# Optimization experiments

Measured on AMD Instinct MI355X. Metric: run time of the kernel, lower is better.

Reference implementation:

```python
import jax, jax.numpy as jnp
import numpy as np

K = 4096
D = 64
DECAY = 0.99
EPS = 1e-05


def setup_inputs() -> dict:
    key = jax.random.key(0)
    k1, k2 = jax.random.split(key)
    z_e = jax.random.normal(k1, (32, 1024, D), dtype=jnp.float32)
    emb = jax.random.normal(k2, (K, D), dtype=jnp.float32)
    emb = emb / jnp.clip(jnp.linalg.norm(emb, axis=1, keepdims=True), 1e-8)
    return {
        "z_e": z_e,
        "embedding": emb,
        "ema_cluster_size": jnp.zeros((K,), jnp.float32),
        "ema_embedding": jnp.zeros((K, D), jnp.float32),
    }


def reference(z_e, embedding, ema_cluster_size, ema_embedding):
    B, L, Dd = z_e.shape
    flat = z_e.reshape(-1, Dd)                                   # (N, D)
    flat_norm = flat / jnp.clip(jnp.linalg.norm(flat, axis=1, keepdims=True), 1e-8)
    dots = flat_norm @ embedding.T                               # (N, K)
    indices = jnp.argmax(dots, axis=1)                           # (N,)
    z_q = embedding[indices].reshape(B, L, Dd)
    z_q_st = z_e + jax.lax.stop_gradient(z_q - z_e)

    # ---- usage / stats ----
    usage = jnp.zeros((K,), jnp.float32).at[indices].add(1.0)    # bincount
    probs = usage / jnp.maximum(usage.sum(), 1.0)
    safe = jnp.where(probs > 0, probs, 1.0)
    perplexity = jnp.exp(-jnp.sum(probs * jnp.log(safe)))
    dead_ratio = jnp.mean((usage == 0).astype(jnp.float32))
    stats = jnp.stack([perplexity, dead_ratio])

    # ---- EMA update (training-mode buffer math, functional) ----
    fn = jax.lax.stop_gradient(flat_norm)
    embed_sum = jnp.zeros((K, Dd), jnp.float32).at[indices].add(fn)  # one_hot.T @ flat_norm
    new_cs = DECAY * ema_cluster_size + (1.0 - DECAY) * usage
    new_ema_emb = DECAY * ema_embedding + (1.0 - DECAY) * embed_sum
    n = new_cs.sum()
    smoothed = (new_cs + EPS) / (n + K * EPS)
    norm_e = new_ema_emb / jnp.clip(smoothed, EPS)[:, None]
    norm_e = norm_e / jnp.clip(jnp.linalg.norm(norm_e, axis=1, keepdims=True), 1e-8)

    # ---- dead-code reinit (reinit_prob=1.0, threshold=0); deterministic key ----
    N = fn.shape[0]
    rand_idx = jax.random.randint(jax.random.key(1), (K,), 0, N)
    src = fn[rand_idx]
    src = src / jnp.clip(jnp.linalg.norm(src, axis=1, keepdims=True), 1e-8)
    dead = usage <= 0.0
    new_embedding = jnp.where(dead[:, None], src, norm_e)

    return (z_q_st, z_q, indices.reshape(B, L), stats,
            new_embedding, new_cs, new_ema_emb)
```

## Files before the change

### kernel.cpp

```cpp
#include <hip/hip_runtime.h>
#include <math.h>

#define N_TOK 32768
#define KCB   4096
#define SPLITS 6

#define OFF_ZQST   0
#define OFF_ZQ     2097152
#define OFF_IDX    4194304
#define OFF_STATS  4227072
#define OFF_NEWEMB 4227074
#define OFF_NEWCS  4489218
#define OFF_NEWEMA 4493314

#define WS_FN       0
#define WS_ESUM     8388608
#define WS_USAGE    9437184
#define WS_CNTS     9453568
#define WS_FULLKEY  9454592
#define WS_EHI      9716736
#define WS_ELO      10241024
#define WS_PK1      10765312
#define WS_PK2      11551744
#define WS_IDXW     12338176
#define WS_RIDX     12469248
#define WS_FULL     12485632

#define THRKEY 131072u
#define DGRKEY 98304u

typedef __attribute__((ext_vector_type(8))) short short8;
typedef __attribute__((ext_vector_type(4))) float float4v;

__device__ __forceinline__ float wave_sum(float v) {
#pragma unroll
  for (int off = 32; off > 0; off >>= 1) v += __shfl_xor(v, off, 64);
  return v;
}

__device__ __forceinline__ unsigned short f2bf(float f) {
  unsigned u = __float_as_uint(f);
  unsigned r = (u + 0x7fffu + ((u >> 16) & 1u)) >> 16;
  return (unsigned short)r;
}
__device__ __forceinline__ float bf2f(unsigned short h) {
  return __uint_as_float(((unsigned)h) << 16);
}

__device__ __forceinline__ unsigned rotl32(unsigned x, int d) {
  return (x << d) | (x >> (32 - d));
}
__device__ __forceinline__ void tf2x32(unsigned k0, unsigned k1,
                                       unsigned x0, unsigned x1,
                                       unsigned& o0, unsigned& o1) {
  unsigned ks2 = k0 ^ k1 ^ 0x1BD11BDAu;
  unsigned v0 = x0 + k0, v1 = x1 + k1;
  v0 += v1; v1 = rotl32(v1, 13) ^ v0;
  v0 += v1; v1 = rotl32(v1, 15) ^ v0;
  v0 += v1; v1 = rotl32(v1, 26) ^ v0;
  v0 += v1; v1 = rotl32(v1, 6) ^ v0;
  v0 += k1; v1 += ks2 + 1u;
  v0 += v1; v1 = rotl32(v1, 17) ^ v0;
  v0 += v1; v1 = rotl32(v1, 29) ^ v0;
  v0 += v1; v1 = rotl32(v1, 16) ^ v0;
  v0 += v1; v1 = rotl32(v1, 24) ^ v0;
  v0 += ks2; v1 += k0 + 2u;
  v0 += v1; v1 = rotl32(v1, 13) ^ v0;
  v0 += v1; v1 = rotl32(v1, 15) ^ v0;
  v0 += v1; v1 = rotl32(v1, 26) ^ v0;
  v0 += v1; v1 = rotl32(v1, 6) ^ v0;
  v0 += k0; v1 += k1 + 3u;
  v0 += v1; v1 = rotl32(v1, 17) ^ v0;
  v0 += v1; v1 = rotl32(v1, 29) ^ v0;
  v0 += v1; v1 = rotl32(v1, 16) ^ v0;
  v0 += v1; v1 = rotl32(v1, 24) ^ v0;
  v0 += k1; v1 += ks2 + 4u;
  v0 += v1; v1 = rotl32(v1, 13) ^ v0;
  v0 += v1; v1 = rotl32(v1, 15) ^ v0;
  v0 += v1; v1 = rotl32(v1, 26) ^ v0;
  v0 += v1; v1 = rotl32(v1, 6) ^ v0;
  v0 += ks2; v1 += k0 + 5u;
  o0 = v0; o1 = v1;
}

__global__ __launch_bounds__(256) void k_prep(const float* __restrict__ z_e,
                                              const float* __restrict__ emb,
                                              float* __restrict__ fn,
                                              unsigned short* __restrict__ ehi,
                                              unsigned short* __restrict__ elo,
                                              int* __restrict__ ridx,
                                              int* __restrict__ zbase) {
  int b = blockIdx.x;
  int t = threadIdx.x;
  if (b < 8192) {
    int n = b * 4 + (t >> 6);
    int lane = t & 63;
    float x = z_e[n * 64 + lane];
    float ss = wave_sum(x * x);
    fn[n * 64 + lane] = x / fmaxf(sqrtf(ss), 1e-8f);
  } else if (b < 9216) {
    int i = (b - 8192) * 256 + t;
    float x = emb[i];
    unsigned short h = f2bf(x);
    ehi[i] = h;
    elo[i] = f2bf(x - bf2f(h));
  } else if (b < 9224) {
    int j = (b - 9216) * 256 + t;
    unsigned a0, b0, a1, b1;
    tf2x32(0u, 1u, 0u, 2u, a0, b0);
    tf2x32(0u, 1u, 1u, 3u, a1, b1);
    unsigned o0, o1;
    tf2x32(b0, b1, (unsigned)j, (unsigned)(j + 2048), o0, o1);
    ridx[j] = (int)(o0 & 32767u);
    ridx[j + 2048] = (int)(o1 & 32767u);
  } else {
    int i = (b - 9224) * 256 + t;
    zbase[i] = 0;
  }
}

__global__ __launch_bounds__(256, 3) void k_dots(const float* __restrict__ fn,
                                                 const unsigned short* __restrict__ ehi,
                                                 const unsigned short* __restrict__ elo,
                                                 unsigned* __restrict__ pk1,
                                                 unsigned* __restrict__ pk2) {
  int t = threadIdx.x;
  int wave = t >> 6, lane = t & 63;
  int g = lane >> 4, n = lane & 15;
  int qw = blockIdx.x * 256 + wave * 64;
  int split = blockIdx.y;
  int nt16 = (split < 2) ? 704 : 672;
  int tstart16 = (split < 3) ? 704 * split : 672 * split + 64;
  int ntiles = nt16 >> 4;

  short8 ahi[4][2], alo[4][2];
#pragma unroll
  for (int s = 0; s < 4; s++)
#pragma unroll
    for (int ks = 0; ks < 2; ks++) {
      const float* src = fn + (qw + s * 16 + n) * 64 + ks * 32 + g * 8;
      short8 h, l;
#pragma unroll
      for (int j = 0; j < 8; j++) {
        float f = src[j] * 0.125f;
        unsigned short hu = f2bf(f);
        h[j] = (short)hu;
        l[j] = (short)f2bf(f - bf2f(hu));
      }
      ahi[s][ks] = h;
      alo[s][ks] = l;
    }

  unsigned run1[4][4], run2[4][4];
#pragma unroll
  for (int s = 0; s < 4; s++)
#pragma unroll
    for (int r = 0; r < 4; r++) { run1[s][r] = 0u; run2[s][r] = 0u; }

  const unsigned short* bh = ehi + (tstart16 + n) * 64 + g * 8;
  const unsigned short* bl = elo + (tstart16 + n) * 64 + g * 8;
  const float hiclamp = __uint_as_float(0x3F9FFFFFu);

  short8 h0a = *(const short8*)(bh);
  short8 h1a = *(const short8*)(bh + 32);
  short8 l0a = *(const short8*)(bl);
  short8 l1a = *(const short8*)(bl + 32);
  short8 h0b = *(const short8*)(bh + 1024);
  short8 h1b = *(const short8*)(bh + 1024 + 32);
  short8 l0b = *(const short8*)(bl + 1024);
  short8 l1b = *(const short8*)(bl + 1024 + 32);

#define MFMA_BLOCK(H0, H1, L0, L1)                                              \
    float4v a0 = (float4v){1.125f, 1.125f, 1.125f, 1.125f};                     \
    float4v a1 = a0, a2 = a0, a3 = a0;                                          \
    a0 = __builtin_amdgcn_mfma_f32_16x16x32_bf16(alo[0][0], H0, a0, 0, 0, 0);   \
    a1 = __builtin_amdgcn_mfma_f32_16x16x32_bf16(alo[1][0], H0, a1, 0, 0, 0);   \
    a2 = __builtin_amdgcn_mfma_f32_16x16x32_bf16(alo[2][0], H0, a2, 0, 0, 0);   \
    a3 = __builtin_amdgcn_mfma_f32_16x16x32_bf16(alo[3][0], H0, a3, 0, 0, 0);   \
    a0 = __builtin_amdgcn_mfma_f32_16x16x32_bf16(alo[0][1], H1, a0, 0, 0, 0);   \
    a1 = __builtin_amdgcn_mfma_f32_16x16x32_bf16(alo[1][1], H1, a1, 0, 0, 0);   \
    a2 = __builtin_amdgcn_mfma_f32_16x16x32_bf16(alo[2][1], H1, a2, 0, 0, 0);   \
    a3 = __builtin_amdgcn_mfma_f32_16x16x32_bf16(alo[3][1], H1, a3, 0, 0, 0);   \
    a0 = __builtin_amdgcn_mfma_f32_16x16x32_bf16(ahi[0][0], L0, a0, 0, 0, 0);   \
    a1 = __builtin_amdgcn_mfma_f32_16x16x32_bf16(ahi[1][0], L0, a1, 0, 0, 0);   \
    a2 = __builtin_amdgcn_mfma_f32_16x16x32_bf16(ahi[2][0], L0, a2, 0, 0, 0);   \
    a3 = __builtin_amdgcn_mfma_f32_16x16x32_bf16(ahi[3][0], L0, a3, 0, 0, 0);   \
    a0 = __builtin_amdgcn_mfma_f32_16x16x32_bf16(ahi[0][1], L1, a0, 0, 0, 0);   \
    a1 = __builtin_amdgcn_mfma_f32_16x16x32_bf16(ahi[1][1], L1, a1, 0, 0, 0);   \
    a2 = __builtin_amdgcn_mfma_f32_16x16x32_bf16(ahi[2][1], L1, a2, 0, 0, 0);   \
    a3 = __builtin_amdgcn_mfma_f32_16x16x32_bf16(ahi[3][1], L1, a3, 0, 0, 0);   \
    a0 = __builtin_amdgcn_mfma_f32_16x16x32_bf16(ahi[0][0], H0, a0, 0, 0, 0);   \
    a1 = __builtin_amdgcn_mfma_f32_16x16x32_bf16(ahi[1][0], H0, a1, 0, 0, 0);   \
    a2 = __builtin_amdgcn_mfma_f32_16x16x32_bf16(ahi[2][0], H0, a2, 0, 0, 0);   \
    a3 = __builtin_amdgcn_mfma_f32_16x16x32_bf16(ahi[3][0], H0, a3, 0, 0, 0);   \
    a0 = __builtin_amdgcn_mfma_f32_16x16x32_bf16(ahi[0][1], H1, a0, 0, 0, 0);   \
    a1 = __builtin_amdgcn_mfma_f32_16x16x32_bf16(ahi[1][1], H1, a1, 0, 0, 0);   \
    a2 = __builtin_amdgcn_mfma_f32_16x16x32_bf16(ahi[2][1], H1, a2, 0, 0, 0);   \
    a3 = __builtin_amdgcn_mfma_f32_16x16x32_bf16(ahi[3][1], H1, a3, 0, 0, 0);

#define SELECT_BLOCK(KT)                                                        \
    {                                                                           \
      unsigned invb = (unsigned)(nt16 - 1 - (KT) * 16 - n);                     \
      _Pragma("unroll") for (int r = 0; r < 4; r++) {                           \
        float x0 = __builtin_amdgcn_fmed3f(a0[r], 1.0f, hiclamp);               \
        unsigned kb0 = (__float_as_uint(x0) << 10) + invb;                      \
        run2[0][r] = max(run2[0][r], min(run1[0][r], kb0));                     \
        run1[0][r] = max(run1[0][r], kb0);                                      \
        float x1 = __builtin_amdgcn_fmed3f(a1[r], 1.0f, hiclamp);               \
        unsigned kb1 = (__float_as_uint(x1) << 10) + invb;                      \
        run2[1][r] = max(run2[1][r], min(run1[1][r], kb1));                     \
        run1[1][r] = max(run1[1][r], kb1);                                      \
        float x2 = __builtin_amdgcn_fmed3f(a2[r], 1.0f, hiclamp);               \
        unsigned kb2 = (__float_as_uint(x2) << 10) + invb;                      \
        run2[2][r] = max(run2[2][r], min(run1[2][r], kb2));                     \
        run1[2][r] = max(run1[2][r], kb2);                                      \
        float x3 = __builtin_amdgcn_fmed3f(a3[r], 1.0f, hiclamp);               \
        unsigned kb3 = (__float_as_uint(x3) << 10) + invb;                      \
        run2[3][r] = max(run2[3][r], min(run1[3][r], kb3));                     \
        run1[3][r] = max(run1[3][r], kb3);                                      \
      }                                                                         \
    }

#pragma unroll 1
  for (int kt = 0; kt < ntiles; kt += 2) {
    {
      MFMA_BLOCK(h0a, h1a, l0a, l1a)
      int off = (kt + 2) * 1024;
      h0a = *(const short8*)(bh + off);
      h1a = *(const short8*)(bh + off + 32);
      l0a = *(const short8*)(bl + off);
      l1a = *(const short8*)(bl + off + 32);
      SELECT_BLOCK(kt)
    }
    {
      MFMA_BLOCK(h0b, h1b, l0b, l1b)
      int off = (kt + 3) * 1024;
      h0b = *(const short8*)(bh + off);
      h1b = *(const short8*)(bh + off + 32);
      l0b = *(const short8*)(bl + off);
      l1b = *(const short8*)(bl + off + 32);
      SELECT_BLOCK(kt + 1)
    }
  }
#undef MFMA_BLOCK
#undef SELECT_BLOCK

#pragma unroll
  for (int off = 1; off <= 8; off <<= 1) {
#pragma unroll
    for (int s = 0; s < 4; s++)
#pragma unroll
      for (int r = 0; r < 4; r++) {
        unsigned o1 = (unsigned)__shfl_xor((int)run1[s][r], off, 64);
        unsigned o2 = (unsigned)__shfl_xor((int)run2[s][r], off, 64);
        run2[s][r] = max(min(run1[s][r], o1), max(run2[s][r], o2));
        run1[s][r] = max(run1[s][r], o1);
      }
  }

  if (n == 0) {
#pragma unroll
    for (int s = 0; s < 4; s++)
#pragma unroll
      for (int r = 0; r < 4; r++) {
        int q = qw + s * 16 + g * 4 + r;
        pk1[split * N_TOK + q] = run1[s][r];
        pk2[split * N_TOK + q] = run2[s][r];
      }
  }
}

__global__ __launch_bounds__(256) void k_merge_fix(const unsigned* __restrict__ pk1,
                                                   const unsigned* __restrict__ pk2,
                                                   const float* __restrict__ fn,
                                                   const float* __restrict__ emb,
                                                   int* __restrict__ idxw,
                                                   int* __restrict__ cnts,
                                                   int* __restrict__ full,
                                                   unsigned long long* __restrict__ fullkey) {
  __shared__ int nfl;
  __shared__ int fl[256][13];
  int t = threadIdx.x;
  if (t == 0) nfl = 0;
  __syncthreads();
  int q = blockIdx.x * 256 + t;
  unsigned k1v[SPLITS], k2v[SPLITS];
  unsigned b1 = 0u, b2 = 0u;
  int s1 = 0;
#pragma unroll
  for (int s = 0; s < SPLITS; s++) {
    unsigned k1 = pk1[s * N_TOK + q];
    unsigned k2 = pk2[s * N_TOK + q];
    k1v[s] = k1;
    k2v[s] = k2;
    b2 = max(b2, min(b1, k1));
    b2 = max(b2, k2);
    if (k1 > b1) { b1 = k1; s1 = s; }
  }
  int nt16s = (s1 < 2) ? 704 : 672;
  int ts16 = (s1 < 3) ? 704 * s1 : 672 * s1 + 64;
  idxw[q] = ts16 + nt16s - 1 - (int)(b1 & 1023u);
  fullkey[q] = 0ull;
  bool danger = false;
#pragma unroll
  for (int s = 0; s < SPLITS; s++) danger |= (k2v[s] + DGRKEY > b1);
  if (danger) {
    int p = atomicAdd(&cnts[0], 1);
    full[p] = q;
  } else if (b1 - b2 < THRKEY) {
    int p = atomicAdd(&nfl, 1);
    fl[p][0] = q;
#pragma unroll
    for (int s = 0; s < SPLITS; s++) {
      int nt = (s < 2) ? 704 : 672;
      int tss = (s < 3) ? 704 * s : 672 * s + 64;
      fl[p][1 + s] = tss + nt - 1 - (int)(k1v[s] & 1023u);
      fl[p][7 + s] = tss + nt - 1 - (int)(k2v[s] & 1023u);
    }
  }
  __syncthreads();
  int m = nfl;
  int wave = t >> 6, lane = t & 63;
  int c = lane >> 2, dg = lane & 3;
  for (int i = wave; i < m; i += 4) {
    int fq = fl[i][0];
    int code = (c < 12) ? fl[i][1 + c] : fl[i][1];
    const float* er = emb + code * 64 + dg * 16;
    const float* fr = fn + fq * 64 + dg * 16;
    double d = 0.0;
#pragma unroll
    for (int k = 0; k < 16; k++) d += (double)er[k] * (double)fr[k];
    d += __shfl_xor(d, 1, 64);
    d += __shfl_xor(d, 2, 64);
    unsigned long long key =
        ((unsigned long long)__double_as_longlong(d + 2.0) & ~0xFFFULL) |
        (unsigned long long)(4095 - code);
    if (c >= 12) key = 0ull;
#pragma unroll
    for (int off = 4; off <= 32; off <<= 1) {
      unsigned long long o = __shfl_xor(key, off, 64);
      key = key > o ? key : o;
    }
    if (lane == 0) idxw[fq] = 4095 - (int)(key & 0xFFFULL);
  }
}

__global__ __launch_bounds__(256) void k_fix_full(const int* __restrict__ cnts,
                                                  const int* __restrict__ full,
                                                  const float* __restrict__ fn,
                                                  const float* __restrict__ emb,
                                                  unsigned long long* __restrict__ fullkey) {
  __shared__ float sfn[64];
  __shared__ unsigned long long red[256];
  int t = threadIdx.x;
  int total = cnts[0] * 16;
  for (int w = blockIdx.x; w < total; w += gridDim.x) {
    int q = full[w >> 4];
    int c = (w & 15) * 256 + t;
    __syncthreads();
    if (t < 64) sfn[t] = fn[q * 64 + t];
    __syncthreads();
    const float* er = emb + c * 64;
    double s0 = 0, s1 = 0, s2 = 0, s3 = 0;
    for (int k = 0; k < 16; k++) {
      s0 += (double)er[k] * (double)sfn[k];
      s1 += (double)er[k + 16] * (double)sfn[k + 16];
      s2 += (double)er[k + 32] * (double)sfn[k + 32];
      s3 += (double)er[k + 48] * (double)sfn[k + 48];
    }
    double d = (s0 + s1) + (s2 + s3);
    unsigned long long key =
        ((unsigned long long)__double_as_longlong(d + 2.0) & ~0xFFFULL) |
        (unsigned long long)(4095 - c);
    red[t] = key;
    __syncthreads();
    for (int s = 128; s > 0; s >>= 1) {
      if (t < s) red[t] = red[t] > red[t + s] ? red[t] : red[t + s];
      __syncthreads();
    }
    if (t == 0) atomicMax(&fullkey[q], red[0]);
  }
}

__global__ __launch_bounds__(256) void k_write_scatter(const int* __restrict__ idxw,
                                                       const unsigned long long* __restrict__ fullkey,
                                                       const float* __restrict__ z_e,
                                                       const float* __restrict__ emb,
                                                       const float* __restrict__ fn,
                                                       float* __restrict__ out,
                                                       float* __restrict__ esum,
                                                       float* __restrict__ usage) {
  int t = threadIdx.x;
  int nn = blockIdx.x * 4 + (t >> 6);
  int lane = t & 63;
  unsigned long long fk = fullkey[nn];
  int bi = fk ? (4095 - (int)(fk & 0xFFFULL)) : idxw[nn];
  float v = emb[bi * 64 + lane];
  float ze = z_e[nn * 64 + lane];
  out[OFF_ZQST + nn * 64 + lane] = ze + (v - ze);
  out[OFF_ZQ + nn * 64 + lane] = v;
  atomicAdd(&esum[bi * 64 + lane], fn[nn * 64 + lane]);
  if (lane == 0) {
    out[OFF_IDX + nn] = (float)bi;
    atomicAdd(&usage[bi], 1.0f);
  }
}

__global__ __launch_bounds__(256) void k_stats(const float* __restrict__ usage,
                                               const float* __restrict__ ema_cs,
                                               float* __restrict__ scal) {
  __shared__ float rE[4], rD[4], rC[4];
  int t = threadIdx.x;
  int i = blockIdx.x * 256 + t;
  float u = usage[i];
  float p = u * (1.0f / 32768.0f);
  float ent = (p > 0.f) ? p * logf(p) : 0.f;
  float dead = (u == 0.f) ? 1.f : 0.f;
  float cs = 0.99f * ema_cs[i] + 0.01f * u;
  ent = wave_sum(ent);
  dead = wave_sum(dead);
  cs = wave_sum(cs);
  int w = t >> 6, lane = t & 63;
  if (lane == 0) { rE[w] = ent; rD[w] = dead; rC[w] = cs; }
  __syncthreads();
  if (t == 0) {
    atomicAdd(&scal[0], rE[0] + rE[1] + rE[2] + rE[3]);
    atomicAdd(&scal[1], rD[0] + rD[1] + rD[2] + rD[3]);
    atomicAdd(&scal[2], rC[0] + rC[1] + rC[2] + rC[3]);
  }
}

__global__ __launch_bounds__(256) void k_final(const float* __restrict__ usage,
                                               const float* __restrict__ ema_cs,
                                               const float* __restrict__ ema_emb,
                                               const float* __restrict__ esum,
                                               const float* __restrict__ fn,
                                               const int* __restrict__ ridx,
                                               const float* __restrict__ scal,
                                               float* __restrict__ out) {
  int t = threadIdx.x;
  int k = blockIdx.x * 4 + (t >> 6);
  int lane = t & 63;
  if (blockIdx.x == 0 && t == 0) {
    out[OFF_STATS + 0] = expf(-scal[0]);
    out[OFF_STATS + 1] = scal[1] * (1.0f / 4096.0f);
  }
  float u = usage[k];
  float ncs = 0.99f * ema_cs[k] + 0.01f * u;
  if (lane == 0) out[OFF_NEWCS + k] = ncs;
  float nee = 0.99f * ema_emb[k * 64 + lane] + 0.01f * esum[k * 64 + lane];
  out[OFF_NEWEMA + k * 64 + lane] = nee;

  float n = scal[2];
  float smoothed = (ncs + 1e-5f) / (n + 4096.0f * 1e-5f);
  float ne = nee / fmaxf(smoothed, 1e-5f);
  float ss = wave_sum(ne * ne);
  ne = ne / fmaxf(sqrtf(ss), 1e-8f);

  float res;
  if (u <= 0.f) {
    int rsrc = ridx[k];
    float v = fn[rsrc * 64 + lane];
    float s2 = wave_sum(v * v);
    res = v / fmaxf(sqrtf(s2), 1e-8f);
  } else {
    res = ne;
  }
  out[OFF_NEWEMB + k * 64 + lane] = res;
}

extern "C" void kernel_launch(void* const* d_in, const int* in_sizes, int n_in,
                              void* d_out, int out_size, void* d_ws, size_t ws_size,
                              hipStream_t stream) {
  const float* z_e = (const float*)d_in[0];
  const float* emb = (const float*)d_in[1];
  const float* ema_cs = (const float*)d_in[2];
  const float* ema_emb = (const float*)d_in[3];
  float* out = (float*)d_out;
  char* ws = (char*)d_ws;

  float* fn = (float*)(ws + WS_FN);
  float* esum = (float*)(ws + WS_ESUM);
  float* usage = (float*)(ws + WS_USAGE);
  int* cnts = (int*)(ws + WS_CNTS);
  float* scal = (float*)(ws + WS_CNTS + 16);
  unsigned long long* fullkey = (unsigned long long*)(ws + WS_FULLKEY);
  unsigned short* ehi = (unsigned short*)(ws + WS_EHI);
  unsigned short* elo = (unsigned short*)(ws + WS_ELO);
  unsigned* pk1 = (unsigned*)(ws + WS_PK1);
  unsigned* pk2 = (unsigned*)(ws + WS_PK2);
  int* idxw = (int*)(ws + WS_IDXW);
  int* ridx = (int*)(ws + WS_RIDX);
  int* full = (int*)(ws + WS_FULL);

  k_prep<<<10265, 256, 0, stream>>>(z_e, emb, fn, ehi, elo, ridx, (int*)(ws + WS_ESUM));
  k_dots<<<dim3(128, SPLITS), 256, 0, stream>>>(fn, ehi, elo, pk1, pk2);
  k_merge_fix<<<128, 256, 0, stream>>>(pk1, pk2, fn, emb, idxw, cnts, full, fullkey);
  k_fix_full<<<512, 256, 0, stream>>>(cnts, full, fn, emb, fullkey);
  k_write_scatter<<<8192, 256, 0, stream>>>(idxw, fullkey, z_e, emb, fn, out, esum, usage);
  k_stats<<<16, 256, 0, stream>>>(usage, ema_cs, scal);
  k_final<<<1024, 256, 0, stream>>>(usage, ema_cs, ema_emb, esum, fn, ridx, scal, out);
}
```

Before: 173.5 us.

## Replace split-bf16 dot products with split-int8 MFMA and integer keys

```diff
diff --git a/kernel.cpp b/kernel.cpp
--- a/kernel.cpp
+++ b/kernel.cpp
@@ -18,19 +18,18 @@
 #define WS_USAGE    9437184
 #define WS_CNTS     9453568
 #define WS_FULLKEY  9454592
-#define WS_EHI      9716736
-#define WS_ELO      10241024
-#define WS_PK1      10765312
-#define WS_PK2      11551744
-#define WS_IDXW     12338176
-#define WS_RIDX     12469248
-#define WS_FULL     12485632
-
-#define THRKEY 131072u
-#define DGRKEY 98304u
-
-typedef __attribute__((ext_vector_type(8))) short short8;
-typedef __attribute__((ext_vector_type(4))) float float4v;
+#define WS_E8H      9716736
+#define WS_E8L      9978880
+#define WS_PK1      10241024
+#define WS_PK2      11027456
+#define WS_IDXW     11813888
+#define WS_RIDX     11944960
+#define WS_FULL     11961344
+
+#define THRKEY 1100000u
+#define DGRKEY 1100000u
+
+typedef __attribute__((ext_vector_type(4))) int int4v;
 
 __device__ __forceinline__ float wave_sum(float v) {
 #pragma unroll
@@ -38,13 +37,18 @@
   return v;
 }
 
-__device__ __forceinline__ unsigned short f2bf(float f) {
-  unsigned u = __float_as_uint(f);
-  unsigned r = (u + 0x7fffu + ((u >> 16) & 1u)) >> 16;
-  return (unsigned short)r;
-}
-__device__ __forceinline__ float bf2f(unsigned short h) {
-  return __uint_as_float(((unsigned)h) << 16);
+__device__ __forceinline__ int2 q4(float4 v) {
+  int hb = 0, lb = 0;
+  float x[4] = {v.x, v.y, v.z, v.w};
+#pragma unroll
+  for (int j = 0; j < 4; j++) {
+    int q = (int)rintf(x[j] * 16383.0f);
+    int h = q >> 7;
+    int l = q - (h << 7);
+    hb |= (h & 255) << (8 * j);
+    lb |= (l & 255) << (8 * j);
+  }
+  return make_int2(hb, lb);
 }
 
 __device__ __forceinline__ unsigned rotl32(unsigned x, int d) {
@@ -86,8 +90,8 @@
 __global__ __launch_bounds__(256) void k_prep(const float* __restrict__ z_e,
                                               const float* __restrict__ emb,
                                               float* __restrict__ fn,
-                                              unsigned short* __restrict__ ehi,
-                                              unsigned short* __restrict__ elo,
+                                              signed char* __restrict__ e8h,
+                                              signed char* __restrict__ e8l,
                                               int* __restrict__ ridx,
                                               int* __restrict__ zbase) {
   int b = blockIdx.x;
@@ -101,9 +105,10 @@
   } else if (b < 9216) {
     int i = (b - 8192) * 256 + t;
     float x = emb[i];
-    unsigned short h = f2bf(x);
-    ehi[i] = h;
-    elo[i] = f2bf(x - bf2f(h));
+    int q = (int)rintf(x * 16383.0f);
+    int h = q >> 7;
+    e8h[i] = (signed char)h;
+    e8l[i] = (signed char)(q - (h << 7));
   } else if (b < 9224) {
     int j = (b - 9216) * 256 + t;
     unsigned a0, b0, a1, b1;
@@ -120,8 +125,8 @@
 }
 
 __global__ __launch_bounds__(256, 3) void k_dots(const float* __restrict__ fn,
-                                                 const unsigned short* __restrict__ ehi,
-                                                 const unsigned short* __restrict__ elo,
+                                                 const signed char* __restrict__ e8h,
+                                                 const signed char* __restrict__ e8l,
                                                  unsigned* __restrict__ pk1,
                                                  unsigned* __restrict__ pk2) {
   int t = threadIdx.x;
@@ -133,112 +138,97 @@
   int tstart16 = (split < 3) ? 704 * split : 672 * split + 64;
   int ntiles = nt16 >> 4;
 
-  short8 ahi[4][2], alo[4][2];
+  int4v ah0, al0, ah1, al1, ah2, al2, ah3, al3;
+#define LOADA(AH, AL, S)                                     \
+  {                                                          \
+    const float* src = fn + (qw + (S) * 16 + n) * 64 + g * 16; \
+    int2 p0 = q4(*(const float4*)(src));                     \
+    int2 p1 = q4(*(const float4*)(src + 4));                 \
+    int2 p2 = q4(*(const float4*)(src + 8));                 \
+    int2 p3 = q4(*(const float4*)(src + 12));                \
+    AH = (int4v){p0.x, p1.x, p2.x, p3.x};                    \
+    AL = (int4v){p0.y, p1.y, p2.y, p3.y};                    \
+  }
+  LOADA(ah0, al0, 0)
+  LOADA(ah1, al1, 1)
+  LOADA(ah2, al2, 2)
+  LOADA(ah3, al3, 3)
+#undef LOADA
+
+  unsigned run1[4][4], run2[4][4];
 #pragma unroll
   for (int s = 0; s < 4; s++)
 #pragma unroll
-    for (int ks = 0; ks < 2; ks++) {
-      const float* src = fn + (qw + s * 16 + n) * 64 + ks * 32 + g * 8;
-      short8 h, l;
-#pragma unroll
-      for (int j = 0; j < 8; j++) {
-        float f = src[j] * 0.125f;
-        unsigned short hu = f2bf(f);
-        h[j] = (short)hu;
-        l[j] = (short)f2bf(f - bf2f(hu));
-      }
-      ahi[s][ks] = h;
-      alo[s][ks] = l;
-    }
-
-  unsigned run1[4][4], run2[4][4];
-#pragma unroll
-  for (int s = 0; s < 4; s++)
-#pragma unroll
     for (int r = 0; r < 4; r++) { run1[s][r] = 0u; run2[s][r] = 0u; }
 
-  const unsigned short* bh = ehi + (tstart16 + n) * 64 + g * 8;
-  const unsigned short* bl = elo + (tstart16 + n) * 64 + g * 8;
-  const float hiclamp = __uint_as_float(0x3F9FFFFFu);
-
-  short8 h0a = *(const short8*)(bh);
-  short8 h1a = *(const short8*)(bh + 32);
-  short8 l0a = *(const short8*)(bl);
-  short8 l1a = *(const short8*)(bl + 32);
-  short8 h0b = *(const short8*)(bh + 1024);
-  short8 h1b = *(const short8*)(bh + 1024 + 32);
-  short8 l0b = *(const short8*)(bl + 1024);
-  short8 l1b = *(const short8*)(bl + 1024 + 32);
-
-#define MFMA_BLOCK(H0, H1, L0, L1)                                              \
-    float4v a0 = (float4v){1.125f, 1.125f, 1.125f, 1.125f};                     \
-    float4v a1 = a0, a2 = a0, a3 = a0;                                          \
-    a0 = __builtin_amdgcn_mfma_f32_16x16x32_bf16(alo[0][0], H0, a0, 0, 0, 0);   \
-    a1 = __builtin_amdgcn_mfma_f32_16x16x32_bf16(alo[1][0], H0, a1, 0, 0, 0);   \
-    a2 = __builtin_amdgcn_mfma_f32_16x16x32_bf16(alo[2][0], H0, a2, 0, 0, 0);   \
-    a3 = __builtin_amdgcn_mfma_f32_16x16x32_bf16(alo[3][0], H0, a3, 0, 0, 0);   \
-    a0 = __builtin_amdgcn_mfma_f32_16x16x32_bf16(alo[0][1], H1, a0, 0, 0, 0);   \
-    a1 = __builtin_amdgcn_mfma_f32_16x16x32_bf16(alo[1][1], H1, a1, 0, 0, 0);   \
-    a2 = __builtin_amdgcn_mfma_f32_16x16x32_bf16(alo[2][1], H1, a2, 0, 0, 0);   \
-    a3 = __builtin_amdgcn_mfma_f32_16x16x32_bf16(alo[3][1], H1, a3, 0, 0, 0);   \
-    a0 = __builtin_amdgcn_mfma_f32_16x16x32_bf16(ahi[0][0], L0, a0, 0, 0, 0);   \
-    a1 = __builtin_amdgcn_mfma_f32_16x16x32_bf16(ahi[1][0], L0, a1, 0, 0, 0);   \
-    a2 = __builtin_amdgcn_mfma_f32_16x16x32_bf16(ahi[2][0], L0, a2, 0, 0, 0);   \
-    a3 = __builtin_amdgcn_mfma_f32_16x16x32_bf16(ahi[3][0], L0, a3, 0, 0, 0);   \
-    a0 = __builtin_amdgcn_mfma_f32_16x16x32_bf16(ahi[0][1], L1, a0, 0, 0, 0);   \
-    a1 = __builtin_amdgcn_mfma_f32_16x16x32_bf16(ahi[1][1], L1, a1, 0, 0, 0);   \
-    a2 = __builtin_amdgcn_mfma_f32_16x16x32_bf16(ahi[2][1], L1, a2, 0, 0, 0);   \
-    a3 = __builtin_amdgcn_mfma_f32_16x16x32_bf16(ahi[3][1], L1, a3, 0, 0, 0);   \
-    a0 = __builtin_amdgcn_mfma_f32_16x16x32_bf16(ahi[0][0], H0, a0, 0, 0, 0);   \
-    a1 = __builtin_amdgcn_mfma_f32_16x16x32_bf16(ahi[1][0], H0, a1, 0, 0, 0);   \
-    a2 = __builtin_amdgcn_mfma_f32_16x16x32_bf16(ahi[2][0], H0, a2, 0, 0, 0);   \
-    a3 = __builtin_amdgcn_mfma_f32_16x16x32_bf16(ahi[3][0], H0, a3, 0, 0, 0);   \
-    a0 = __builtin_amdgcn_mfma_f32_16x16x32_bf16(ahi[0][1], H1, a0, 0, 0, 0);   \
-    a1 = __builtin_amdgcn_mfma_f32_16x16x32_bf16(ahi[1][1], H1, a1, 0, 0, 0);   \
-    a2 = __builtin_amdgcn_mfma_f32_16x16x32_bf16(ahi[2][1], H1, a2, 0, 0, 0);   \
-    a3 = __builtin_amdgcn_mfma_f32_16x16x32_bf16(ahi[3][1], H1, a3, 0, 0, 0);
-
-#define SELECT_BLOCK(KT)                                                        \
-    {                                                                           \
-      unsigned invb = (unsigned)(nt16 - 1 - (KT) * 16 - n);                     \
-      _Pragma("unroll") for (int r = 0; r < 4; r++) {                           \
-        float x0 = __builtin_amdgcn_fmed3f(a0[r], 1.0f, hiclamp);               \
-        unsigned kb0 = (__float_as_uint(x0) << 10) + invb;                      \
-        run2[0][r] = max(run2[0][r], min(run1[0][r], kb0));                     \
-        run1[0][r] = max(run1[0][r], kb0);                                      \
-        float x1 = __builtin_amdgcn_fmed3f(a1[r], 1.0f, hiclamp);               \
-        unsigned kb1 = (__float_as_uint(x1) << 10) + invb;                      \
-        run2[1][r] = max(run2[1][r], min(run1[1][r], kb1));                     \
-        run1[1][r] = max(run1[1][r], kb1);                                      \
-        float x2 = __builtin_amdgcn_fmed3f(a2[r], 1.0f, hiclamp);               \
-        unsigned kb2 = (__float_as_uint(x2) << 10) + invb;                      \
-        run2[2][r] = max(run2[2][r], min(run1[2][r], kb2));                     \
-        run1[2][r] = max(run1[2][r], kb2);                                      \
-        float x3 = __builtin_amdgcn_fmed3f(a3[r], 1.0f, hiclamp);               \
-        unsigned kb3 = (__float_as_uint(x3) << 10) + invb;                      \
-        run2[3][r] = max(run2[3][r], min(run1[3][r], kb3));                     \
-        run1[3][r] = max(run1[3][r], kb3);                                      \
-      }                                                                         \
+  const signed char* bhp = e8h + (tstart16 + n) * 64 + g * 16;
+  const signed char* blp = e8l + (tstart16 + n) * 64 + g * 16;
+
+  int4v hA = *(const int4v*)(bhp);
+  int4v lA = *(const int4v*)(blp);
+  int4v hB = *(const int4v*)(bhp + 1024);
+  int4v lB = *(const int4v*)(blp + 1024);
+
+#define MFMA_BLOCK(BH, BL)                                                     \
+    int4v hh0 = (int4v){16480, 16480, 16480, 16480};                           \
+    int4v hh1 = hh0, hh2 = hh0, hh3 = hh0;                                     \
+    int4v mm0 = (int4v){0, 0, 0, 0};                                           \
+    int4v mm1 = mm0, mm2 = mm0, mm3 = mm0;                                     \
+    int4v ll0 = mm0, ll1 = mm0, ll2 = mm0, ll3 = mm0;                          \
+    hh0 = __builtin_amdgcn_mfma_i32_16x16x64_i8(ah0, BH, hh0, 0, 0, 0);        \
+    hh1 = __builtin_amdgcn_mfma_i32_16x16x64_i8(ah1, BH, hh1, 0, 0, 0);        \
+    hh2 = __builtin_amdgcn_mfma_i32_16x16x64_i8(ah2, BH, hh2, 0, 0, 0);        \
+    hh3 = __builtin_amdgcn_mfma_i32_16x16x64_i8(ah3, BH, hh3, 0, 0, 0);        \
+    mm0 = __builtin_amdgcn_mfma_i32_16x16x64_i8(ah0, BL, mm0, 0, 0, 0);        \
+    mm1 = __builtin_amdgcn_mfma_i32_16x16x64_i8(ah1, BL, mm1, 0, 0, 0);        \
+    mm2 = __builtin_amdgcn_mfma_i32_16x16x64_i8(ah2, BL, mm2, 0, 0, 0);        \
+    mm3 = __builtin_amdgcn_mfma_i32_16x16x64_i8(ah3, BL, mm3, 0, 0, 0);        \
+    mm0 = __builtin_amdgcn_mfma_i32_16x16x64_i8(al0, BH, mm0, 0, 0, 0);        \
+    mm1 = __builtin_amdgcn_mfma_i32_16x16x64_i8(al1, BH, mm1, 0, 0, 0);        \
+    mm2 = __builtin_amdgcn_mfma_i32_16x16x64_i8(al2, BH, mm2, 0, 0, 0);        \
+    mm3 = __builtin_amdgcn_mfma_i32_16x16x64_i8(al3, BH, mm3, 0, 0, 0);        \
+    ll0 = __builtin_amdgcn_mfma_i32_16x16x64_i8(al0, BL, ll0, 0, 0, 0);        \
+    ll1 = __builtin_amdgcn_mfma_i32_16x16x64_i8(al1, BL, ll1, 0, 0, 0);        \
+    ll2 = __builtin_amdgcn_mfma_i32_16x16x64_i8(al2, BL, ll2, 0, 0, 0);        \
+    ll3 = __builtin_amdgcn_mfma_i32_16x16x64_i8(al3, BL, ll3, 0, 0, 0);
+
+#define SELECT_BLOCK(KT)                                                       \
+    {                                                                          \
+      unsigned invb = (unsigned)(nt16 - 1 - (KT) * 16 - n);                    \
+      _Pragma("unroll") for (int r = 0; r < 4; r++) {                          \
+        unsigned dq0 = (unsigned)((((hh0[r] << 7) + mm0[r]) << 7) + ll0[r]);   \
+        unsigned kb0 = ((dq0 >> 8) << 10) + invb;                              \
+        run2[0][r] = max(run2[0][r], min(run1[0][r], kb0));                    \
+        run1[0][r] = max(run1[0][r], kb0);                                     \
+        unsigned dq1 = (unsigned)((((hh1[r] << 7) + mm1[r]) << 7) + ll1[r]);   \
+        unsigned kb1 = ((dq1 >> 8) << 10) + invb;                              \
+        run2[1][r] = max(run2[1][r], min(run1[1][r], kb1));                    \
+        run1[1][r] = max(run1[1][r], kb1);                                     \
+        unsigned dq2 = (unsigned)((((hh2[r] << 7) + mm2[r]) << 7) + ll2[r]);   \
+        unsigned kb2 = ((dq2 >> 8) << 10) + invb;                              \
+        run2[2][r] = max(run2[2][r], min(run1[2][r], kb2));                    \
+        run1[2][r] = max(run1[2][r], kb2);                                     \
+        unsigned dq3 = (unsigned)((((hh3[r] << 7) + mm3[r]) << 7) + ll3[r]);   \
+        unsigned kb3 = ((dq3 >> 8) << 10) + invb;                              \
+        run2[3][r] = max(run2[3][r], min(run1[3][r], kb3));                    \
+        run1[3][r] = max(run1[3][r], kb3);                                     \
+      }                                                                        \
     }
 
 #pragma unroll 1
   for (int kt = 0; kt < ntiles; kt += 2) {
     {
-      MFMA_BLOCK(h0a, h1a, l0a, l1a)
+      MFMA_BLOCK(hA, lA)
       int off = (kt + 2) * 1024;
-      h0a = *(const short8*)(bh + off);
-      h1a = *(const short8*)(bh + off + 32);
-      l0a = *(const short8*)(bl + off);
-      l1a = *(const short8*)(bl + off + 32);
+      hA = *(const int4v*)(bhp + off);
+      lA = *(const int4v*)(blp + off);
       SELECT_BLOCK(kt)
     }
     {
-      MFMA_BLOCK(h0b, h1b, l0b, l1b)
+      MFMA_BLOCK(hB, lB)
       int off = (kt + 3) * 1024;
-      h0b = *(const short8*)(bh + off);
-      h1b = *(const short8*)(bh + off + 32);
-      l0b = *(const short8*)(bl + off);
-      l1b = *(const short8*)(bl + off + 32);
+      hB = *(const int4v*)(bhp + off);
+      lB = *(const int4v*)(blp + off);
       SELECT_BLOCK(kt + 1)
     }
   }
@@ -485,16 +475,16 @@
   int* cnts = (int*)(ws + WS_CNTS);
   float* scal = (float*)(ws + WS_CNTS + 16);
   unsigned long long* fullkey = (unsigned long long*)(ws + WS_FULLKEY);
-  unsigned short* ehi = (unsigned short*)(ws + WS_EHI);
-  unsigned short* elo = (unsigned short*)(ws + WS_ELO);
+  signed char* e8h = (signed char*)(ws + WS_E8H);
+  signed char* e8l = (signed char*)(ws + WS_E8L);
   unsigned* pk1 = (unsigned*)(ws + WS_PK1);
   unsigned* pk2 = (unsigned*)(ws + WS_PK2);
   int* idxw = (int*)(ws + WS_IDXW);
   int* ridx = (int*)(ws + WS_RIDX);
   int* full = (int*)(ws + WS_FULL);
 
-  k_prep<<<10265, 256, 0, stream>>>(z_e, emb, fn, ehi, elo, ridx, (int*)(ws + WS_ESUM));
-  k_dots<<<dim3(128, SPLITS), 256, 0, stream>>>(fn, ehi, elo, pk1, pk2);
+  k_prep<<<10265, 256, 0, stream>>>(z_e, emb, fn, e8h, e8l, ridx, (int*)(ws + WS_ESUM));
+  k_dots<<<dim3(128, SPLITS), 256, 0, stream>>>(fn, e8h, e8l, pk1, pk2);
   k_merge_fix<<<128, 256, 0, stream>>>(pk1, pk2, fn, emb, idxw, cnts, full, fullkey);
   k_fix_full<<<512, 256, 0, stream>>>(cnts, full, fn, emb, fullkey);
   k_write_scatter<<<8192, 256, 0, stream>>>(idxw, fullkey, z_e, emb, fn, out, esum, usage);
```

Measured after the change: 197.7 us. +13.9%, slower.
